# Kernel tuning notes

Hardware: AMD Instinct MI355X
Metric: run time of the kernel (lower is better)

## Reference

```python
import jax, jax.numpy as jnp
import numpy as np

NUM_HEAD = 16
D_MODEL = 1024


def setup_inputs() -> dict:
    key = jax.random.key(0)
    k1, k2, k3 = jax.random.split(key, 3)
    B, S = 4, 2048
    x = jax.random.normal(k1, (B, S, D_MODEL), dtype=jnp.float32)
    W_qkv = jax.random.normal(k2, (D_MODEL, 3 * D_MODEL), dtype=jnp.float32) * (D_MODEL ** -0.5)
    b_qkv = jnp.zeros((3 * D_MODEL,), dtype=jnp.float32)
    W_o = jax.random.normal(k3, (D_MODEL, D_MODEL), dtype=jnp.float32) * (D_MODEL ** -0.5)
    b_o = jnp.zeros((D_MODEL,), dtype=jnp.float32)
    return {"x": x, "W_qkv": W_qkv, "b_qkv": b_qkv, "W_o": W_o, "b_o": b_o}


def reference(x, W_qkv, b_qkv, W_o, b_o):
    B, S, dm = x.shape
    H = NUM_HEAD
    hd = dm // H
    qkv = x @ W_qkv + b_qkv                       # [B,S,3*dm]
    qkv = qkv.reshape(B, S, H, 3 * hd).transpose(0, 2, 1, 3)  # [B,H,S,3*hd]
    q, k, v = jnp.split(qkv, 3, axis=-1)          # each [B,H,S,hd]
    scale = jnp.sqrt(jnp.asarray(hd, dtype=q.dtype))
    att = jnp.einsum('bhqd,bhkd->bhqk', q, k) / scale  # [B,H,S,S]
    causal = jnp.tril(jnp.ones((S, S), dtype=bool))    # band_part(ones,-1,0)
    att = jnp.where(causal, att, -jnp.inf)             # additive 0 / -inf mask
    att = jax.nn.softmax(att, axis=-1)
    vals = jnp.einsum('bhqk,bhkd->bhqd', att, v)       # [B,H,S,hd]
    # Faithful to original: reshape WITHOUT transposing heads back (axis scramble)
    vals = vals.reshape(B, S, H * hd)
    return vals @ W_o + b_o
```

## Files before the change

kernel.cpp:

```cpp
#include <hip/hip_runtime.h>
#include <hip/hip_bf16.h>
#include <stdint.h>


typedef __attribute__((ext_vector_type(8))) __bf16 bf16x8;
typedef __attribute__((ext_vector_type(4))) float f32x4;
typedef __attribute__((ext_vector_type(16))) float f32x16;

#define AS_G __attribute__((address_space(1)))
#define AS_L __attribute__((address_space(3)))

__device__ __forceinline__ void gload_lds16(const void* g, void* s) {
  __builtin_amdgcn_global_load_lds((const AS_G void*)g, (AS_L void*)s, 16, 0, 0);
}

__device__ __forceinline__ unsigned cvt_pk_bf16(float lo, float hi) {
  unsigned r;
  asm("v_cvt_pk_bf16_f32 %0, %1, %2" : "=v"(r) : "v"(lo), "v"(hi));
  return r;
}

__global__ void cvt_bf16_kernel(const float* __restrict__ in,
                                __bf16* __restrict__ out, int n8) {
  int i = blockIdx.x * blockDim.x + threadIdx.x;
  if (i >= n8) return;
  float4 a = ((const float4*)in)[i * 2];
  float4 b = ((const float4*)in)[i * 2 + 1];
  union { __bf16 h[8]; int4 v; } u;
  u.h[0] = (__bf16)a.x; u.h[1] = (__bf16)a.y; u.h[2] = (__bf16)a.z; u.h[3] = (__bf16)a.w;
  u.h[4] = (__bf16)b.x; u.h[5] = (__bf16)b.y; u.h[6] = (__bf16)b.z; u.h[7] = (__bf16)b.w;
  ((int4*)out)[i] = u.v;
}

__global__ void cvt_T_kernel(const float* __restrict__ in,
                             __bf16* __restrict__ out, int K, int N) {
  __shared__ float tile[32][33];
  int bx = blockIdx.x;
  int by = blockIdx.y;
  int tx = threadIdx.x & 31, ty = threadIdx.x >> 5;
#pragma unroll
  for (int i = 0; i < 32; i += 8)
    tile[ty + i][tx] = in[(size_t)(by * 32 + ty + i) * N + bx * 32 + tx];
  __syncthreads();
#pragma unroll
  for (int i = 0; i < 32; i += 8)
    out[(size_t)(bx * 32 + ty + i) * K + by * 32 + tx] = (__bf16)tile[tx][ty + i];
}

template <int MODE>
__global__ __launch_bounds__(256) void gemm_bt(
    const __bf16* __restrict__ A, const __bf16* __restrict__ Bt,
    const float* __restrict__ bias,
    __bf16* __restrict__ Qb, __bf16* __restrict__ Kb, __bf16* __restrict__ Vtb,
    float* __restrict__ Out) {
  __shared__ __bf16 As[128 * 32];
  __shared__ __bf16 Bs[128 * 32];
  const int tid = threadIdx.x;
  const int wave = tid >> 6, lane = tid & 63;
  const int lhi = lane >> 4, llo = lane & 15;
  const int wm = wave >> 1, wn = wave & 1;
  const int m0 = blockIdx.y * 128, n0 = blockIdx.x * 128;

  const int srow = lane >> 2;
  const int scol = (lane & 3) * 8;
  const __bf16* Ag0 = A + (size_t)(m0 + (wave * 2 + 0) * 16 + srow) * 1024 + scol;
  const __bf16* Ag1 = A + (size_t)(m0 + (wave * 2 + 1) * 16 + srow) * 1024 + scol;
  const __bf16* Bg0 = Bt + (size_t)(n0 + (wave * 2 + 0) * 16 + srow) * 1024 + scol;
  const __bf16* Bg1 = Bt + (size_t)(n0 + (wave * 2 + 1) * 16 + srow) * 1024 + scol;
  __bf16* As0 = As + (wave * 2 + 0) * 512;
  __bf16* As1 = As + (wave * 2 + 1) * 512;
  __bf16* Bs0 = Bs + (wave * 2 + 0) * 512;
  __bf16* Bs1 = Bs + (wave * 2 + 1) * 512;

  f32x4 acc[4][4];
#pragma unroll
  for (int m = 0; m < 4; ++m)
#pragma unroll
    for (int n = 0; n < 4; ++n) acc[m][n] = (f32x4){0.f, 0.f, 0.f, 0.f};

  for (int k0 = 0; k0 < 1024; k0 += 32) {
    gload_lds16(Ag0 + k0, As0);
    gload_lds16(Ag1 + k0, As1);
    gload_lds16(Bg0 + k0, Bs0);
    gload_lds16(Bg1 + k0, Bs1);
    __syncthreads();
    bf16x8 af[4], bfr[4];
#pragma unroll
    for (int i = 0; i < 4; ++i)
      af[i] = *(const bf16x8*)&As[(wm * 64 + i * 16 + llo) * 32 + lhi * 8];
#pragma unroll
    for (int i = 0; i < 4; ++i)
      bfr[i] = *(const bf16x8*)&Bs[(wn * 64 + i * 16 + llo) * 32 + lhi * 8];
#pragma unroll
    for (int m = 0; m < 4; ++m)
#pragma unroll
      for (int n = 0; n < 4; ++n)
        acc[m][n] = __builtin_amdgcn_mfma_f32_16x16x32_bf16(af[m], bfr[n],
                                                            acc[m][n], 0, 0, 0);
    __syncthreads();
  }

#pragma unroll
  for (int ni = 0; ni < 4; ++ni) {
    const int col = n0 + wn * 64 + ni * 16 + llo;
    const float bv = bias[col];
    if (MODE == 0) {
      const int h = col / 192, rem = col % 192;
#pragma unroll
      for (int mi = 0; mi < 4; ++mi) {
        const int row0 = m0 + wm * 64 + mi * 16 + lhi * 4;
        const int b = row0 >> 11;
        const int s0 = row0 & 2047;
        const int bh = b * 16 + h;
        f32x4 v = acc[mi][ni];
        if (rem < 64) {
#pragma unroll
          for (int r = 0; r < 4; ++r)
            Qb[((size_t)bh * 2048 + s0 + r) * 64 + rem] =
                (__bf16)((v[r] + bv) * 0.18033688011112042f);
        } else if (rem < 128) {
#pragma unroll
          for (int r = 0; r < 4; ++r)
            Kb[((size_t)bh * 2048 + s0 + r) * 64 + (rem - 64)] = (__bf16)(v[r] + bv);
        } else {
          union { __bf16 h4[4]; int2 v2; } u;
#pragma unroll
          for (int r = 0; r < 4; ++r) u.h4[r] = (__bf16)(v[r] + bv);
          *(int2*)&Vtb[((size_t)bh * 64 + (rem - 128)) * 2048 + s0] = u.v2;
        }
      }
    } else {
#pragma unroll
      for (int mi = 0; mi < 4; ++mi) {
        const int row0 = m0 + wm * 64 + mi * 16 + lhi * 4;
        f32x4 v = acc[mi][ni];
#pragma unroll
        for (int r = 0; r < 4; ++r)
          Out[(size_t)(row0 + r) * 1024 + col] = v[r] + bv;
      }
    }
  }
}


__device__ __forceinline__ void attn_tile(
    const __bf16* __restrict__ ksb, const __bf16* __restrict__ vsb,
    const bf16x8* qf, int kv0, int q0w, int lq, int hi,
    f32x16& o0, f32x16& o1, float& m, float& l) {
  const int r0 = lq, r1 = 32 + lq;
  const int fx = (lq & 7) ^ ((lq >> 3) << 1);
  f32x16 s0, s1;
#pragma unroll
  for (int i = 0; i < 16; ++i) { s0[i] = 0.f; s1[i] = 0.f; }
  __builtin_amdgcn_s_setprio(1);
#pragma unroll
  for (int ds = 0; ds < 4; ++ds) {
    const int bb = ((ds * 2 + hi) ^ fx) * 8;
    bf16x8 k0 = *(const bf16x8*)&ksb[r0 * 64 + bb];
    bf16x8 k1 = *(const bf16x8*)&ksb[r1 * 64 + bb];
    s0 = __builtin_amdgcn_mfma_f32_32x32x16_bf16(k0, qf[ds], s0, 0, 0, 0);
    s1 = __builtin_amdgcn_mfma_f32_32x32x16_bf16(k1, qf[ds], s1, 0, 0, 0);
  }
  __builtin_amdgcn_s_setprio(0);

  const int qg = q0w + lq;
  if (kv0 + 63 > q0w) {
#pragma unroll
    for (int reg = 0; reg < 16; ++reg) {
      const int kvl = (reg & 3) + 8 * (reg >> 2) + 4 * hi;
      if (kv0 + kvl > qg) s0[reg] = -1e30f;
      if (kv0 + 32 + kvl > qg) s1[reg] = -1e30f;
    }
  }
  float x[8];
#pragma unroll
  for (int i = 0; i < 8; ++i)
    x[i] = fmaxf(fmaxf(s0[i], s0[i + 8]), fmaxf(s1[i], s1[i + 8]));
#pragma unroll
  for (int st = 4; st; st >>= 1)
#pragma unroll
    for (int i = 0; i < st; ++i) x[i] = fmaxf(x[i], x[i + st]);
  const float mx = fmaxf(x[0], __shfl_xor(x[0], 32));

  if (!__all(mx <= m + 8.f)) {
    const float mn = fmaxf(m, mx);
    const float f = __builtin_amdgcn_exp2f(m - mn);
    m = mn;
    l *= f;
#pragma unroll
    for (int i = 0; i < 16; ++i) { o0[i] *= f; o1[i] *= f; }
  }
#pragma unroll
  for (int i = 0; i < 16; ++i) s0[i] = __builtin_amdgcn_exp2f(s0[i] - m);
#pragma unroll
  for (int i = 0; i < 16; ++i) s1[i] = __builtin_amdgcn_exp2f(s1[i] - m);
  float y[8];
#pragma unroll
  for (int i = 0; i < 8; ++i) y[i] = (s0[i] + s0[i + 8]) + (s1[i] + s1[i + 8]);
#pragma unroll
  for (int st = 4; st; st >>= 1)
#pragma unroll
    for (int i = 0; i < st; ++i) y[i] += y[i + st];
  l += y[0] + __shfl_xor(y[0], 32);

#pragma unroll
  for (int ks = 0; ks < 4; ++ks) {
    unsigned pa, pb, pc, pd;
    if (ks < 2) {
      pa = cvt_pk_bf16(s0[ks * 8 + 0], s0[ks * 8 + 1]);
      pb = cvt_pk_bf16(s0[ks * 8 + 2], s0[ks * 8 + 3]);
      pc = cvt_pk_bf16(s0[ks * 8 + 4], s0[ks * 8 + 5]);
      pd = cvt_pk_bf16(s0[ks * 8 + 6], s0[ks * 8 + 7]);
    } else {
      pa = cvt_pk_bf16(s1[(ks - 2) * 8 + 0], s1[(ks - 2) * 8 + 1]);
      pb = cvt_pk_bf16(s1[(ks - 2) * 8 + 2], s1[(ks - 2) * 8 + 3]);
      pc = cvt_pk_bf16(s1[(ks - 2) * 8 + 4], s1[(ks - 2) * 8 + 5]);
      pd = cvt_pk_bf16(s1[(ks - 2) * 8 + 6], s1[(ks - 2) * 8 + 7]);
    }
    asm volatile("v_permlane32_swap_b32 %0, %1" : "+v"(pa), "+v"(pc));
    asm volatile("v_permlane32_swap_b32 %0, %1" : "+v"(pb), "+v"(pd));
    union { unsigned u[4]; bf16x8 v; } pf;
    pf.u[0] = pa; pf.u[1] = pb; pf.u[2] = pc; pf.u[3] = pd;
    const int vb = ((ks * 2 + hi) ^ fx) * 8;
    bf16x8 v0 = *(const bf16x8*)&vsb[r0 * 64 + vb];
    bf16x8 v1 = *(const bf16x8*)&vsb[r1 * 64 + vb];
    o0 = __builtin_amdgcn_mfma_f32_32x32x16_bf16(v0, pf.v, o0, 0, 0, 0);
    o1 = __builtin_amdgcn_mfma_f32_32x32x16_bf16(v1, pf.v, o1, 0, 0, 0);
  }
}

__device__ __forceinline__ void attn_epilogue(
    __bf16* __restrict__ vals, int bh, int q0w, int lq, int hi,
    const f32x16& o0, const f32x16& o1, float l) {
  const float inv = 1.f / l;
  unsigned* outp = (unsigned*)(vals + ((size_t)bh * 2048 + q0w + lq) * 64);
#pragma unroll
  for (int n = 0; n < 2; ++n) {
#pragma unroll
    for (int g = 0; g < 2; ++g) {
      const float e0 = (n ? o1[g * 8 + 0] : o0[g * 8 + 0]) * inv;
      const float e1 = (n ? o1[g * 8 + 1] : o0[g * 8 + 1]) * inv;
      const float e2 = (n ? o1[g * 8 + 2] : o0[g * 8 + 2]) * inv;
      const float e3 = (n ? o1[g * 8 + 3] : o0[g * 8 + 3]) * inv;
      const float e4 = (n ? o1[g * 8 + 4] : o0[g * 8 + 4]) * inv;
      const float e5 = (n ? o1[g * 8 + 5] : o0[g * 8 + 5]) * inv;
      const float e6 = (n ? o1[g * 8 + 6] : o0[g * 8 + 6]) * inv;
      const float e7 = (n ? o1[g * 8 + 7] : o0[g * 8 + 7]) * inv;
      unsigned a = cvt_pk_bf16(e0, e1);
      unsigned a2 = cvt_pk_bf16(e2, e3);
      unsigned b = cvt_pk_bf16(e4, e5);
      unsigned b2 = cvt_pk_bf16(e6, e7);
      asm volatile("v_permlane32_swap_b32 %0, %1" : "+v"(a), "+v"(b));
      asm volatile("v_permlane32_swap_b32 %0, %1" : "+v"(a2), "+v"(b2));
      int4 st = {(int)a, (int)a2, (int)b, (int)b2};
      *(int4*)&outp[(n * 32 + g * 16 + hi * 8) >> 1] = st;
    }
  }
}

__global__ __launch_bounds__(256) void attn_kernel(
    const __bf16* __restrict__ Q, const __bf16* __restrict__ K,
    const __bf16* __restrict__ Vt, __bf16* __restrict__ vals) {
  __shared__ __bf16 Ks[2][4096];
  __shared__ __bf16 Vs[2][4096];
  const int tid = threadIdx.x;
  const int wave = tid >> 6, lane = tid & 63;
  const int lq = lane & 31, hi = lane >> 5;

  const int wg = blockIdx.x + (blockIdx.y << 3);
  const int wgid = (wg & 7) * 128 + (wg >> 3);
  const int local = wgid & 127;
  const int bh = (wgid >> 7) * 8 + (local & 7);
  const int qc = 15 - (local >> 3);
  const int q0w = qc * 128 + wave * 32;
  const int nt = 2 * qc + 2;

  bf16x8 qf[4];
  {
    const __bf16* qp = Q + ((size_t)bh * 2048 + q0w + lq) * 64 + hi * 8;
#pragma unroll
    for (int ds = 0; ds < 4; ++ds) qf[ds] = *(const bf16x8*)(qp + ds * 16);
  }

  f32x16 o0, o1;
#pragma unroll
  for (int i = 0; i < 16; ++i) { o0[i] = 0.f; o1[i] = 0.f; }
  float m = -3e38f, l = 0.f;

  const int sr = tid >> 3, sb_ = tid & 7;
  const int sc = (sb_ ^ ((sr & 7) ^ ((sr >> 3) << 1))) * 8;
  const __bf16* Kg0 = K + ((size_t)bh * 2048 + sr) * 64 + sc;
  const __bf16* Kg1 = Kg0 + 32 * 64;
  const __bf16* Vg0 = Vt + ((size_t)bh * 64 + sr) * 2048 + sc;
  const __bf16* Vg1 = Vg0 + 32 * 2048;
  __bf16* KsW = &Ks[0][0] + wave * 512;
  __bf16* VsW = &Vs[0][0] + wave * 512;

#define STAGE(buf, t)                                                   \
  gload_lds16(Kg0 + (size_t)(t) * 4096, KsW + (buf) * 4096);            \
  gload_lds16(Kg1 + (size_t)(t) * 4096, KsW + (buf) * 4096 + 2048);     \
  gload_lds16(Vg0 + (t) * 64, VsW + (buf) * 4096);                      \
  gload_lds16(Vg1 + (t) * 64, VsW + (buf) * 4096 + 2048);

  STAGE(0, 0);
  __syncthreads();

  for (int t = 0; t < nt; ++t) {
    const int cur = t & 1;
    if (t + 1 < nt) { STAGE(cur ^ 1, t + 1); }
    attn_tile(&Ks[cur][0], &Vs[cur][0], qf, t * 64, q0w, lq, hi, o0, o1, m, l);
    __syncthreads();
  }
#undef STAGE

  attn_epilogue(vals, bh, q0w, lq, hi, o0, o1, l);
}

extern "C" void kernel_launch(void* const* d_in, const int* in_sizes, int n_in,
                              void* d_out, int out_size, void* d_ws, size_t ws_size,
                              hipStream_t stream) {
  const float* x = (const float*)d_in[0];
  const float* Wqkv = (const float*)d_in[1];
  const float* bqkv = (const float*)d_in[2];
  const float* Wo = (const float*)d_in[3];
  const float* bo = (const float*)d_in[4];
  float* out = (float*)d_out;
  char* ws = (char*)d_ws;

  __bf16* xb  = (__bf16*)(ws);
  __bf16* Wqt = (__bf16*)(ws + 16777216);
  __bf16* Wot = (__bf16*)(ws + 23068672);
  __bf16* Qb  = (__bf16*)(ws + 25165824);
  __bf16* Kb  = (__bf16*)(ws + 41943040);
  __bf16* Vtb = (__bf16*)(ws + 58720256);
  __bf16* vals = xb;

  cvt_bf16_kernel<<<4096, 256, 0, stream>>>(x, xb, 1048576);
  cvt_T_kernel<<<dim3(96, 32), 256, 0, stream>>>(Wqkv, Wqt, 1024, 3072);
  cvt_T_kernel<<<dim3(32, 32), 256, 0, stream>>>(Wo, Wot, 1024, 1024);
  gemm_bt<0><<<dim3(24, 64), 256, 0, stream>>>(xb, Wqt, bqkv, Qb, Kb, Vtb, nullptr);
  attn_kernel<<<dim3(8, 128), 256, 0, stream>>>(Qb, Kb, Vtb, vals);
  gemm_bt<1><<<dim3(8, 64), 256, 0, stream>>>(vals, Wot, bo, nullptr, nullptr, nullptr, out);
}
```

Measured before the change: 179.0 us.

## Pipeline GEMM loads with double-buffered swizzled LDS and XCD-aware block remap

Rewrites the bf16 GEMM main loop to prefetch K-slices into a 64KB double-buffered, XOR-swizzled LDS layout with K=64 stages split into two 32-wide phases. Global-to-LDS loads for future stages are issued before the MFMA block, with partial vmcnt waits, raised wave priority and sched barriers. Workgroup IDs are remapped across the 8 XCDs for better L2 locality. The aim is to hide memory latency and cut LDS bank conflicts, at the cost of 64KB of LDS per block, which limits occupancy, and fixed K=1024 assumptions.

After: 176.4 us. No clear change (-1.4%).

```diff
diff --git a/kernel.cpp b/kernel.cpp
--- a/kernel.cpp
+++ b/kernel.cpp
@@ -47,62 +47,106 @@
     out[(size_t)(bx * 32 + ty + i) * K + by * 32 + tx] = (__bf16)tile[tx][ty + i];
 }
 
-template <int MODE>
-__global__ __launch_bounds__(256) void gemm_bt(
+template <int MODE, int NT, int NBLK>
+__global__ __launch_bounds__(256, 2) void gemm_bt(
     const __bf16* __restrict__ A, const __bf16* __restrict__ Bt,
     const float* __restrict__ bias,
     __bf16* __restrict__ Qb, __bf16* __restrict__ Kb, __bf16* __restrict__ Vtb,
     float* __restrict__ Out) {
-  __shared__ __bf16 As[128 * 32];
-  __shared__ __bf16 Bs[128 * 32];
+  __shared__ char lds[65536];
   const int tid = threadIdx.x;
   const int wave = tid >> 6, lane = tid & 63;
   const int lhi = lane >> 4, llo = lane & 15;
   const int wm = wave >> 1, wn = wave & 1;
-  const int m0 = blockIdx.y * 128, n0 = blockIdx.x * 128;
-
-  const int srow = lane >> 2;
-  const int scol = (lane & 3) * 8;
-  const __bf16* Ag0 = A + (size_t)(m0 + (wave * 2 + 0) * 16 + srow) * 1024 + scol;
-  const __bf16* Ag1 = A + (size_t)(m0 + (wave * 2 + 1) * 16 + srow) * 1024 + scol;
-  const __bf16* Bg0 = Bt + (size_t)(n0 + (wave * 2 + 0) * 16 + srow) * 1024 + scol;
-  const __bf16* Bg1 = Bt + (size_t)(n0 + (wave * 2 + 1) * 16 + srow) * 1024 + scol;
-  __bf16* As0 = As + (wave * 2 + 0) * 512;
-  __bf16* As1 = As + (wave * 2 + 1) * 512;
-  __bf16* Bs0 = Bs + (wave * 2 + 0) * 512;
-  __bf16* Bs1 = Bs + (wave * 2 + 1) * 512;
+
+  const int wg = blockIdx.x + blockIdx.y * gridDim.x;
+  const int wgid = (wg & 7) * (NBLK >> 3) + (wg >> 3);
+  const int m0 = (wgid / NT) * 128, n0 = (wgid % NT) * 128;
+
+  int S[2];
+#pragma unroll
+  for (int j = 0; j < 2; ++j) {
+    const int idx = j * 256 + tid;
+    const int v = idx >> 3, wl = idx & 7;
+    const int wg_ = wl ^ (v & 7);
+    const int r = (v << 1) | (wg_ >> 2), u2 = wg_ & 3;
+    S[j] = r * 1024 + u2 * 8;
+  }
+  const __bf16* Asrc = A + (size_t)m0 * 1024;
+  const __bf16* Bsrc = Bt + (size_t)n0 * 1024;
+  const int dstw = wave * 1024;
+
+  auto stageAB = [&](int c, int t, int ks) {
+    char* ab = &lds[c * 16384 + ks * 8192];
+    char* bb = &lds[32768 + c * 16384 + ks * 8192];
+    const int go = t * 64 + ks * 32;
+    gload_lds16(Asrc + S[0] + go, ab + dstw);
+    gload_lds16(Asrc + S[1] + go, ab + 4096 + dstw);
+    gload_lds16(Bsrc + S[0] + go, bb + dstw);
+    gload_lds16(Bsrc + S[1] + go, bb + 4096 + dstw);
+  };
 
   f32x4 acc[4][4];
 #pragma unroll
-  for (int m = 0; m < 4; ++m)
-#pragma unroll
-    for (int n = 0; n < 4; ++n) acc[m][n] = (f32x4){0.f, 0.f, 0.f, 0.f};
-
-  for (int k0 = 0; k0 < 1024; k0 += 32) {
-    gload_lds16(Ag0 + k0, As0);
-    gload_lds16(Ag1 + k0, As1);
-    gload_lds16(Bg0 + k0, Bs0);
-    gload_lds16(Bg1 + k0, Bs1);
-    __syncthreads();
-    bf16x8 af[4], bfr[4];
-#pragma unroll
-    for (int i = 0; i < 4; ++i)
-      af[i] = *(const bf16x8*)&As[(wm * 64 + i * 16 + llo) * 32 + lhi * 8];
-#pragma unroll
-    for (int i = 0; i < 4; ++i)
-      bfr[i] = *(const bf16x8*)&Bs[(wn * 64 + i * 16 + llo) * 32 + lhi * 8];
-#pragma unroll
-    for (int m = 0; m < 4; ++m)
-#pragma unroll
-      for (int n = 0; n < 4; ++n)
-        acc[m][n] = __builtin_amdgcn_mfma_f32_16x16x32_bf16(af[m], bfr[n],
-                                                            acc[m][n], 0, 0, 0);
-    __syncthreads();
-  }
-
-#pragma unroll
-  for (int ni = 0; ni < 4; ++ni) {
-    const int col = n0 + wn * 64 + ni * 16 + llo;
+  for (int mi = 0; mi < 4; ++mi)
+#pragma unroll
+    for (int nj = 0; nj < 4; ++nj) acc[mi][nj] = (f32x4){0.f, 0.f, 0.f, 0.f};
+
+  auto aoff = [&](int c, int ks, int mi) {
+    const int r = wm * 64 + mi * 16 + llo;
+    const int v = r >> 1;
+    const int w = ((r & 1) << 2) | lhi;
+    return c * 16384 + ks * 8192 + v * 128 + ((w ^ (v & 7)) << 4);
+  };
+  auto boff = [&](int c, int ks, int nj) {
+    const int r = wn * 64 + nj * 16 + llo;
+    const int v = r >> 1;
+    const int w = ((r & 1) << 2) | lhi;
+    return 32768 + c * 16384 + ks * 8192 + v * 128 + ((w ^ (v & 7)) << 4);
+  };
+
+  auto phase = [&](int c, int ks, int sc, int st, int sks) {
+    bf16x8 fa[4], fb[4];
+#pragma unroll
+    for (int mi = 0; mi < 4; ++mi) fa[mi] = *(const bf16x8*)&lds[aoff(c, ks, mi)];
+#pragma unroll
+    for (int nj = 0; nj < 4; ++nj) fb[nj] = *(const bf16x8*)&lds[boff(c, ks, nj)];
+    stageAB(sc, st, sks);
+    __builtin_amdgcn_sched_barrier(0);
+    asm volatile("s_waitcnt vmcnt(8)" ::: "memory");
+    __builtin_amdgcn_sched_barrier(0);
+    __builtin_amdgcn_s_barrier();
+    __builtin_amdgcn_s_setprio(1);
+#pragma unroll
+    for (int mi = 0; mi < 4; ++mi)
+#pragma unroll
+      for (int nj = 0; nj < 4; ++nj)
+        acc[mi][nj] = __builtin_amdgcn_mfma_f32_16x16x32_bf16(fa[mi], fb[nj],
+                                                              acc[mi][nj], 0, 0, 0);
+    __builtin_amdgcn_s_setprio(0);
+    __builtin_amdgcn_sched_barrier(0);
+    __builtin_amdgcn_s_barrier();
+  };
+
+  stageAB(0, 0, 0);
+  stageAB(0, 0, 1);
+  stageAB(1, 1, 0);
+  __builtin_amdgcn_sched_barrier(0);
+  asm volatile("s_waitcnt vmcnt(8)" ::: "memory");
+  __builtin_amdgcn_sched_barrier(0);
+  __builtin_amdgcn_s_barrier();
+
+  for (int it = 0; it < 8; ++it) {
+    const int T = 2 * it;
+    phase(0, 0, 1, (T + 1) & 15, 1);
+    phase(0, 1, 0, (T + 2) & 15, 0);
+    phase(1, 0, 0, (T + 2) & 15, 1);
+    phase(1, 1, 1, (T + 3) & 15, 0);
+  }
+
+#pragma unroll
+  for (int nj = 0; nj < 4; ++nj) {
+    const int col = n0 + wn * 64 + nj * 16 + llo;
     const float bv = bias[col];
     if (MODE == 0) {
       const int h = col / 192, rem = col % 192;
@@ -112,7 +156,7 @@
         const int b = row0 >> 11;
         const int s0 = row0 & 2047;
         const int bh = b * 16 + h;
-        f32x4 v = acc[mi][ni];
+        f32x4 v = acc[mi][nj];
         if (rem < 64) {
 #pragma unroll
           for (int r = 0; r < 4; ++r)
@@ -133,7 +177,7 @@
 #pragma unroll
       for (int mi = 0; mi < 4; ++mi) {
         const int row0 = m0 + wm * 64 + mi * 16 + lhi * 4;
-        f32x4 v = acc[mi][ni];
+        f32x4 v = acc[mi][nj];
 #pragma unroll
         for (int r = 0; r < 4; ++r)
           Out[(size_t)(row0 + r) * 1024 + col] = v[r] + bv;
@@ -338,7 +382,7 @@
   cvt_bf16_kernel<<<4096, 256, 0, stream>>>(x, xb, 1048576);
   cvt_T_kernel<<<dim3(96, 32), 256, 0, stream>>>(Wqkv, Wqt, 1024, 3072);
   cvt_T_kernel<<<dim3(32, 32), 256, 0, stream>>>(Wo, Wot, 1024, 1024);
-  gemm_bt<0><<<dim3(24, 64), 256, 0, stream>>>(xb, Wqt, bqkv, Qb, Kb, Vtb, nullptr);
+  gemm_bt<0, 24, 1536><<<dim3(24, 64), 256, 0, stream>>>(xb, Wqt, bqkv, Qb, Kb, Vtb, nullptr);
   attn_kernel<<<dim3(8, 128), 256, 0, stream>>>(Qb, Kb, Vtb, vals);
-  gemm_bt<1><<<dim3(8, 64), 256, 0, stream>>>(vals, Wot, bo, nullptr, nullptr, nullptr, out);
-}
+  gemm_bt<1, 8, 512><<<dim3(8, 64), 256, 0, stream>>>(vals, Wot, bo, nullptr, nullptr, nullptr, out);
+}
```
